# Kernel optimization log

Hardware: AMD Instinct MI355X
Metric: run time of the kernel (lower is better)

Reference implementation:

```python
import jax, jax.numpy as jnp
import numpy as np

N, E = 10000, 160000
IN_DIM, HID, HEADS, EDGE_DIM = 1024, 1024, 8, 4
HEAD_DIM = HID // HEADS  # 128
NEG_SLOPE = 0.2
EPS = 1e-16  # PyG softmax denominator epsilon


def _lin(key, fan_in, fan_out, bias=True):
    kw, kb = jax.random.split(key)
    s = 1.0 / np.sqrt(fan_in)
    W = jax.random.uniform(kw, (fan_in, fan_out), minval=-s, maxval=s, dtype=jnp.float32)
    if not bias:
        return W
    b = jax.random.uniform(kb, (fan_out,), minval=-s, maxval=s, dtype=jnp.float32)
    return W, b


def setup_inputs() -> dict:
    key = jax.random.key(0)
    ks = jax.random.split(key, 24)
    x = jax.random.normal(ks[0], (N, IN_DIM), dtype=jnp.float32)
    edge_index = jax.random.randint(ks[1], (2, E), 0, N, dtype=jnp.int64)
    edge_attr = jax.random.normal(ks[2], (E, EDGE_DIM), dtype=jnp.float32)

    W_in, b_in = _lin(ks[3], IN_DIM, HID)

    def gat_params(k):
        k0, k1, k2, k3, k4 = jax.random.split(k, 5)
        Wl, bl = _lin(k0, HID, HID)
        Wr, br = _lin(k1, HID, HID)
        We = _lin(k2, EDGE_DIM, HID, bias=False)
        att = jax.random.normal(k3, (HEADS, HEAD_DIM), dtype=jnp.float32) / np.sqrt(HEAD_DIM)
        b = jnp.zeros((HID,), dtype=jnp.float32)
        return Wl, bl, Wr, br, We, att, b

    g1 = gat_params(ks[4])
    g2 = gat_params(ks[5])
    m1_W, m1_b = _lin(ks[6], HID, 512)
    m2_W, m2_b = _lin(ks[7], 512, 128)
    m3_W, m3_b = _lin(ks[8], 128, 1)

    names1 = ['g1_Wl', 'g1_bl', 'g1_Wr', 'g1_br', 'g1_We', 'g1_att', 'g1_b']
    names2 = ['g2_Wl', 'g2_bl', 'g2_Wr', 'g2_br', 'g2_We', 'g2_att', 'g2_b']
    out = {'x': x, 'edge_index': edge_index, 'edge_attr': edge_attr,
           'W_in': W_in, 'b_in': b_in,
           'm1_W': m1_W, 'm1_b': m1_b, 'm2_W': m2_W, 'm2_b': m2_b,
           'm3_W': m3_W, 'm3_b': m3_b}
    out.update(dict(zip(names1, g1)))
    out.update(dict(zip(names2, g2)))
    return out


def gatv2_layer(x, src, dst, edge_attr, Wl, bl, Wr, br, We, att, bias):
    # x: [N, HID]; returns [N, HID] (heads concatenated)
    xl = (x @ Wl + bl).reshape(-1, HEADS, HEAD_DIM)  # source transform
    xr = (x @ Wr + br).reshape(-1, HEADS, HEAD_DIM)  # target transform
    e = (edge_attr @ We).reshape(-1, HEADS, HEAD_DIM)
    m = jax.nn.leaky_relu(xl[src] + xr[dst] + e, NEG_SLOPE)  # [E, H, D]
    logits = jnp.einsum('ehd,hd->eh', m, att)  # [E, H]
    lmax = jax.ops.segment_max(logits, dst, num_segments=N)
    lmax = jnp.where(jnp.isfinite(lmax), lmax, 0.0)
    ex = jnp.exp(logits - lmax[dst])
    denom = jax.ops.segment_sum(ex, dst, num_segments=N)
    alpha = ex / (denom[dst] + EPS)  # [E, H]
    out = jax.ops.segment_sum(xl[src] * alpha[..., None], dst, num_segments=N)
    return out.reshape(-1, HID) + bias


def reference(x, edge_index, edge_attr, W_in, b_in,
              g1_Wl, g1_bl, g1_Wr, g1_br, g1_We, g1_att, g1_b,
              g2_Wl, g2_bl, g2_Wr, g2_br, g2_We, g2_att, g2_b,
              m1_W, m1_b, m2_W, m2_b, m3_W, m3_b):
    src, dst = edge_index[0], edge_index[1]
    h = jax.nn.elu(x @ W_in + b_in)
    h = jax.nn.elu(gatv2_layer(h, src, dst, edge_attr, g1_Wl, g1_bl, g1_Wr, g1_br, g1_We, g1_att, g1_b))
    h = jax.nn.elu(gatv2_layer(h, src, dst, edge_attr, g2_Wl, g2_bl, g2_Wr, g2_br, g2_We, g2_att, g2_b))
    h = jax.nn.relu(h @ m1_W + m1_b)
    h = jax.nn.relu(h @ m2_W + m2_b)
    return jax.nn.sigmoid(h @ m3_W + m3_b)  # [N, 1]
```

## Files before the change

kernel.cpp:

```cpp
#include <hip/hip_runtime.h>
#include <math.h>

constexpr int HID = 1024;
constexpr float NEG_SLOPE = 0.2f;
constexpr float EPSV = 1e-16f;

typedef __bf16 bf16x8 __attribute__((ext_vector_type(8)));
typedef float f32x4 __attribute__((ext_vector_type(4)));
typedef float f32x2 __attribute__((ext_vector_type(2)));
typedef unsigned short us8 __attribute__((ext_vector_type(8)));
typedef unsigned short us4 __attribute__((ext_vector_type(4)));
typedef unsigned short ushort_t;

#define AS1 __attribute__((address_space(1)))
#define AS3 __attribute__((address_space(3)))

__device__ __forceinline__ float4 ld4(const float* p){ return *reinterpret_cast<const float4*>(p); }
__device__ __forceinline__ float b2f(ushort_t u){ return __uint_as_float(((unsigned)u) << 16); }
__device__ __forceinline__ ushort_t f2b(float f){
  unsigned u = __float_as_uint(f);
  return (ushort_t)((u + 0x7FFFu + ((u >> 16) & 1u)) >> 16);
}
__device__ __forceinline__ float rfl(float x){
  return __uint_as_float(__builtin_amdgcn_readfirstlane(__float_as_uint(x)));
}
__device__ __forceinline__ f32x2 up2(unsigned u){
  f32x2 r;
  r[0] = __uint_as_float(u << 16);
  r[1] = __uint_as_float(u & 0xffff0000u);
  return r;
}
__device__ __forceinline__ f32x2 lrelu2(f32x2 v){
  return __builtin_elementwise_max(v, v * NEG_SLOPE);
}

struct TP5 { const float* src[5]; ushort_t* dst[5]; };
__global__ __launch_bounds__(256) void transpose_f2b_5(TP5 p){
  const int z = blockIdx.z;
  const float* W = p.src[z];
  ushort_t* WT = p.dst[z];
  __shared__ float tile[32][33];
  const int tx = threadIdx.x & 31, ty = threadIdx.x >> 5;
  const int n0 = blockIdx.x * 32, k0 = blockIdx.y * 32;
  #pragma unroll
  for (int r = 0; r < 32; r += 8)
    tile[ty + r][tx] = W[(size_t)(k0 + ty + r) * 1024 + n0 + tx];
  __syncthreads();
  #pragma unroll
  for (int r = 0; r < 32; r += 8)
    WT[(size_t)(n0 + ty + r) * 1024 + k0 + tx] = f2b(tile[tx][ty + r]);
}

__global__ __launch_bounds__(256) void transpose_f2b(const float* __restrict__ W, ushort_t* __restrict__ WT,
                                                     int K, int N){
  __shared__ float tile[32][33];
  const int tx = threadIdx.x & 31, ty = threadIdx.x >> 5;
  const int n0 = blockIdx.x * 32, k0 = blockIdx.y * 32;
  #pragma unroll
  for (int r = 0; r < 32; r += 8)
    tile[ty + r][tx] = W[(size_t)(k0 + ty + r) * N + n0 + tx];
  __syncthreads();
  #pragma unroll
  for (int r = 0; r < 32; r += 8)
    WT[(size_t)(n0 + ty + r) * K + k0 + tx] = f2b(tile[tx][ty + r]);
}

struct BC4 { const float* s[4]; };
__global__ void concat_bias(BC4 p, float* __restrict__ dst){
  const int i = blockIdx.x * blockDim.x + threadIdx.x;
  dst[i] = p.s[i >> 10][i & 1023];
}

__global__ void convert_f2b(const float* __restrict__ in, ushort_t* __restrict__ out, size_t n){
  size_t i = ((size_t)blockIdx.x * blockDim.x + threadIdx.x) * 4;
  const size_t stride = (size_t)gridDim.x * blockDim.x * 4;
  for (; i < n; i += stride){
    const float4 v = ld4(in + i);
    us4 o = {f2b(v.x), f2b(v.y), f2b(v.z), f2b(v.w)};
    *reinterpret_cast<us4*>(out + i) = o;
  }
}

template<int ACT, int OUTB>
__global__ __launch_bounds__(512, 4) void gemm_mfma(
    const ushort_t* __restrict__ A, const ushort_t* __restrict__ BT,
    const float* __restrict__ bias, float* __restrict__ Cf, ushort_t* __restrict__ Cb,
    int M, int K, int N)
{
  __shared__ __align__(16) char smem[65536];
  ushort_t* Asl = (ushort_t*)smem;
  ushort_t* Bsl = (ushort_t*)(smem + 32768);
  const int tid = threadIdx.x;
  const int lane = tid & 63, wave = tid >> 6;
  const int wr = (wave >> 1) * 32;
  const int wc = (wave & 1) * 64;

  const int nwg = gridDim.x * gridDim.y;
  int wg = blockIdx.y * gridDim.x + blockIdx.x;
  {
    const int q = nwg >> 3, r = nwg & 7;
    const int xcd = wg & 7, lo = wg >> 3;
    wg = (xcd < r ? xcd * (q + 1) : r * (q + 1) + (xcd - r) * q) + lo;
  }
  const int bm = (wg / gridDim.x) * 128, bn = (wg % gridDim.x) * 128;

  const int mrow = lane & 15;
  const int r0 = (lane >> 4) * 4;

  f32x4 acc[2][4];
  #pragma unroll
  for (int i = 0; i < 2; ++i)
    #pragma unroll
    for (int j = 0; j < 4; ++j)
      acc[i][j] = (f32x4){0.f, 0.f, 0.f, 0.f};

  const int srow = tid >> 3;
  const int ssl = (((lane & 7) ^ (lane >> 3))) * 8;
  const int ldst = wave * 512 + lane * 8;

  auto stage = [&](int buf, int k0){
    #pragma unroll
    for (int q = 0; q < 2; ++q){
      const int row = q * 64 + srow;
      int arow = bm + row; if (arow > M - 1) arow = M - 1;
      __builtin_amdgcn_global_load_lds(
        (const AS1 unsigned int*)(A + (size_t)arow * K + k0 + ssl),
        (AS3 unsigned int*)(Asl + buf * 8192 + q * 4096 + ldst), 16, 0, 0);
      __builtin_amdgcn_global_load_lds(
        (const AS1 unsigned int*)(BT + (size_t)(bn + row) * K + k0 + ssl),
        (AS3 unsigned int*)(Bsl + buf * 8192 + q * 4096 + ldst), 16, 0, 0);
    }
  };

  const int kslice = (lane >> 4);
  auto compute = [&](int buf){
    #pragma unroll
    for (int ks = 0; ks < 2; ++ks){
      bf16x8 af[2], bfr[4];
      #pragma unroll
      for (int i = 0; i < 2; ++i){
        const int row = wr + i * 16 + mrow;
        const int sl = (ks * 4 + kslice) ^ (row & 7);
        af[i] = *reinterpret_cast<const bf16x8*>(&Asl[buf * 8192 + row * 64 + sl * 8]);
      }
      #pragma unroll
      for (int j = 0; j < 4; ++j){
        const int row = wc + j * 16 + mrow;
        const int sl = (ks * 4 + kslice) ^ (row & 7);
        bfr[j] = *reinterpret_cast<const bf16x8*>(&Bsl[buf * 8192 + row * 64 + sl * 8]);
      }
      #pragma unroll
      for (int i = 0; i < 2; ++i)
        #pragma unroll
        for (int j = 0; j < 4; ++j)
          acc[i][j] = __builtin_amdgcn_mfma_f32_16x16x32_bf16(af[i], bfr[j], acc[i][j], 0, 0, 0);
    }
  };

  const int NT = K >> 6;
  stage(0, 0);
  if (NT > 1) stage(1, 64);

  int cur = 0;
  for (int t = 0; t < NT; ++t){
    if (t + 1 < NT) asm volatile("s_waitcnt vmcnt(4)" ::: "memory");
    else            asm volatile("s_waitcnt vmcnt(0)" ::: "memory");
    __builtin_amdgcn_s_barrier();
    compute(cur);
    __builtin_amdgcn_s_barrier();
    if (t + 2 < NT) stage(cur, (t + 2) << 6);
    cur ^= 1;
  }

  float* ldsF = (float*)smem;
  const int wbase = wave * 2048;
  #pragma unroll
  for (int i = 0; i < 2; ++i)
    #pragma unroll
    for (int j = 0; j < 4; ++j)
      #pragma unroll
      for (int r = 0; r < 4; ++r)
        ldsF[wbase + (i * 16 + r0 + r) * 64 + j * 16 + mrow] = acc[i][j][r];
  asm volatile("s_waitcnt lgkmcnt(0)" ::: "memory");

  const int lrow = lane >> 3, lcol = (lane & 7) * 8;
  #pragma unroll
  for (int i2 = 0; i2 < 4; ++i2){
    const int row = bm + wr + i2 * 8 + lrow;
    const int col = bn + wc + lcol;
    if (row < M){
      const f32x4 lo = *reinterpret_cast<const f32x4*>(&ldsF[wbase + (i2 * 8 + lrow) * 64 + lcol]);
      const f32x4 hi = *reinterpret_cast<const f32x4*>(&ldsF[wbase + (i2 * 8 + lrow) * 64 + lcol + 4]);
      const float4 b0 = ld4(bias + col), b1 = ld4(bias + col + 4);
      float v[8] = {lo[0] + b0.x, lo[1] + b0.y, lo[2] + b0.z, lo[3] + b0.w,
                    hi[0] + b1.x, hi[1] + b1.y, hi[2] + b1.z, hi[3] + b1.w};
      #pragma unroll
      for (int u = 0; u < 8; ++u){
        float t2 = v[u];
        if (ACT == 1) t2 = fmaxf(t2, 0.f);
        else if (ACT == 2) t2 = (t2 > 0.f) ? t2 : expm1f(t2);
        v[u] = t2;
      }
      if (OUTB){
        us8 ov;
        #pragma unroll
        for (int u = 0; u < 8; ++u) ov[u] = f2b(v[u]);
        *reinterpret_cast<us8*>(Cb + (size_t)row * N + col) = ov;
      } else {
        *reinterpret_cast<float4*>(Cf + (size_t)row * N + col)     = make_float4(v[0], v[1], v[2], v[3]);
        *reinterpret_cast<float4*>(Cf + (size_t)row * N + col + 4) = make_float4(v[4], v[5], v[6], v[7]);
      }
    }
  }
}

__global__ void count_deg(const int* __restrict__ dst, int* __restrict__ deg, int E){
  int e = blockIdx.x * blockDim.x + threadIdx.x;
  if (e < E) atomicAdd(&deg[dst[e]], 1);
}

__global__ __launch_bounds__(1024) void scan_offsets(const int* __restrict__ deg, int* __restrict__ offs, int n){
  __shared__ int ws[16];
  const int tid = threadIdx.x, lane = tid & 63, wid = tid >> 6;
  int running = 0;
  for (int base = 0; base < n; base += 1024){
    const int i = base + tid;
    const int v = (i < n) ? deg[i] : 0;
    int x = v;
    #pragma unroll
    for (int s = 1; s < 64; s <<= 1){
      int u = __shfl_up(x, s, 64);
      if (lane >= s) x += u;
    }
    if (lane == 63) ws[wid] = x;
    __syncthreads();
    if (tid < 16){
      int p = ws[tid];
      #pragma unroll
      for (int s = 1; s < 16; s <<= 1){
        int u = __shfl_up(p, s, 64);
        if (tid >= s) p += u;
      }
      ws[tid] = p;
    }
    __syncthreads();
    const int wpre = (wid > 0) ? ws[wid - 1] : 0;
    if (i < n) offs[i] = running + wpre + x - v;
    running += ws[15];
    __syncthreads();
  }
  if (tid == 0) offs[n] = running;
}

__global__ void fill_csr(const int* __restrict__ src, const int* __restrict__ dst,
                         const float* __restrict__ edge_attr,
                         const int* __restrict__ offs, int* __restrict__ cursor,
                         int* __restrict__ csr_src, float* __restrict__ csr_ea, int E){
  int e = blockIdx.x * blockDim.x + threadIdx.x;
  if (e < E){
    int d = dst[e];
    int pos = offs[d] + atomicAdd(&cursor[d], 1);
    csr_src[pos] = src[e];
    *reinterpret_cast<float4*>(csr_ea + (size_t)pos * 4) = ld4(edge_attr + (size_t)e * 4);
  }
}

__global__ __launch_bounds__(128) void fused_gat(
    const int* __restrict__ offs, const int* __restrict__ csr_src, const float* __restrict__ csr_ea,
    const float* __restrict__ We, const float* __restrict__ att,
    const ushort_t* __restrict__ xlr, const float* __restrict__ bias,
    ushort_t* __restrict__ out, int N)
{
  const int n = blockIdx.x;
  const int t = threadIdx.x;
  const int d0 = t * 8;

  f32x2 W0[4], W1[4], W2[4], W3[4], AT[4];
  #pragma unroll
  for (int q = 0; q < 4; ++q){
    W0[q] = *reinterpret_cast<const f32x2*>(We + d0 + 2*q);
    W1[q] = *reinterpret_cast<const f32x2*>(We + 1024 + d0 + 2*q);
    W2[q] = *reinterpret_cast<const f32x2*>(We + 2048 + d0 + 2*q);
    W3[q] = *reinterpret_cast<const f32x2*>(We + 3072 + d0 + 2*q);
    AT[q] = *reinterpret_cast<const f32x2*>(att + d0 + 2*q);
  }
  f32x2 xr[4];
  {
    const uint4 xu = *reinterpret_cast<const uint4*>(xlr + (size_t)n * 2048 + 1024 + d0);
    xr[0] = up2(xu.x); xr[1] = up2(xu.y); xr[2] = up2(xu.z); xr[3] = up2(xu.w);
  }

  const int o0 = __builtin_amdgcn_readfirstlane(offs[n]);
  const int o1 = __builtin_amdgcn_readfirstlane(offs[n + 1]);

  f32x2 acc[4];
  #pragma unroll
  for (int q = 0; q < 4; ++q) acc[q] = (f32x2){0.f, 0.f};
  float lsum = 0.f, mcur = -1e30f;

  uint4 xa = {0u,0u,0u,0u}, xb = {0u,0u,0u,0u};
  float eA0=0.f,eA1=0.f,eA2=0.f,eA3=0.f, eB0=0.f,eB1=0.f,eB2=0.f,eB3=0.f;

  auto ldedge = [&](int idx, uint4& xv, float& e0, float& e1, float& e2, float& e3){
    const int s = __builtin_amdgcn_readfirstlane(csr_src[idx]);
    xv = *reinterpret_cast<const uint4*>(xlr + (size_t)s * 2048 + d0);
    const float4 e = ld4(csr_ea + (size_t)idx * 4);
    e0 = rfl(e.x); e1 = rfl(e.y); e2 = rfl(e.z); e3 = rfl(e.w);
  };

  if (o0 < o1)     ldedge(o0,     xa, eA0,eA1,eA2,eA3);
  if (o0 + 1 < o1) ldedge(o0 + 1, xb, eB0,eB1,eB2,eB3);

  int i = o0;
  while (i < o1){
    const uint4 ca = xa; const float a0=eA0,a1=eA1,a2=eA2,a3=eA3;
    const uint4 cb = xb; const float b0=eB0,b1=eB1,b2=eB2,b3=eB3;
    const bool pair = (i + 1 < o1);
    const int ni = i + 2;
    if (ni < o1)     ldedge(ni,     xa, eA0,eA1,eA2,eA3);
    if (ni + 1 < o1) ldedge(ni + 1, xb, eB0,eB1,eB2,eB3);

    f32x2 xav[4] = {up2(ca.x), up2(ca.y), up2(ca.z), up2(ca.w)};
    f32x2 xbv[4] = {up2(cb.x), up2(cb.y), up2(cb.z), up2(cb.w)};

    f32x2 za2 = {0.f,0.f}, zb2 = {0.f,0.f};
    #pragma unroll
    for (int q = 0; q < 4; ++q){
      f32x2 ma = xav[q] + xr[q];
      ma += W0[q]*a0; ma += W1[q]*a1; ma += W2[q]*a2; ma += W3[q]*a3;
      ma = lrelu2(ma);
      za2 += ma * AT[q];
      f32x2 mb = xbv[q] + xr[q];
      mb += W0[q]*b0; mb += W1[q]*b1; mb += W2[q]*b2; mb += W3[q]*b3;
      mb = lrelu2(mb);
      zb2 += mb * AT[q];
    }
    float zA = za2[0] + za2[1];
    float zB = zb2[0] + zb2[1];
    #pragma unroll
    for (int sh = 1; sh <= 8; sh <<= 1){
      zA += __shfl_xor(zA, sh, 64);
      zB += __shfl_xor(zB, sh, 64);
    }

    if (pair){
      const float mn = fmaxf(fmaxf(mcur, zA), zB);
      const float sc = __expf(mcur - mn);
      const float pA = __expf(zA - mn);
      const float pB = __expf(zB - mn);
      lsum = lsum * sc + pA + pB;
      #pragma unroll
      for (int q = 0; q < 4; ++q)
        acc[q] = acc[q] * sc + xav[q] * pA + xbv[q] * pB;
      mcur = mn;
    } else {
      const float mn = fmaxf(mcur, zA);
      const float sc = __expf(mcur - mn);
      const float pA = __expf(zA - mn);
      lsum = lsum * sc + pA;
      #pragma unroll
      for (int q = 0; q < 4; ++q)
        acc[q] = acc[q] * sc + xav[q] * pA;
      mcur = mn;
    }
    i = ni;
  }

  const float r = 1.f / (lsum + EPSV);
  const float4 bv0 = ld4(bias + d0);
  const float4 bv1 = ld4(bias + d0 + 4);
  float o_[8] = {acc[0][0]*r + bv0.x, acc[0][1]*r + bv0.y, acc[1][0]*r + bv0.z, acc[1][1]*r + bv0.w,
                 acc[2][0]*r + bv1.x, acc[2][1]*r + bv1.y, acc[3][0]*r + bv1.z, acc[3][1]*r + bv1.w};
  us8 ov;
  #pragma unroll
  for (int j = 0; j < 8; ++j){
    float v = o_[j];
    v = (v > 0.f) ? v : expm1f(v);
    ov[j] = f2b(v);
  }
  *reinterpret_cast<us8*>(out + (size_t)n * HID + d0) = ov;
}

__global__ __launch_bounds__(256) void mlp_final(const float* __restrict__ h, const float* __restrict__ w,
                                                 const float* __restrict__ b, float* __restrict__ out, int M)
{
  const int row = (int)((blockIdx.x * (size_t)blockDim.x + threadIdx.x) >> 6);
  const int lane = threadIdx.x & 63;
  if (row >= M) return;
  const float2 v  = *reinterpret_cast<const float2*>(&h[(size_t)row * 128 + lane * 2]);
  const float2 ww = *reinterpret_cast<const float2*>(&w[lane * 2]);
  float s = v.x * ww.x + v.y * ww.y;
  #pragma unroll
  for (int m = 1; m <= 32; m <<= 1) s += __shfl_xor(s, m, 64);
  if (lane == 0) out[row] = 1.f / (1.f + expf(-(s + b[0])));
}

extern "C" void kernel_launch(void* const* d_in, const int* in_sizes, int n_in,
                              void* d_out, int out_size, void* d_ws, size_t ws_size,
                              hipStream_t stream)
{
  const float* x        = (const float*)d_in[0];
  const int*   ei       = (const int*)d_in[1];
  const float* edge_attr= (const float*)d_in[2];
  const float* W_in     = (const float*)d_in[3];
  const float* b_in     = (const float*)d_in[4];
  const float* m1_W     = (const float*)d_in[5];
  const float* m1_b     = (const float*)d_in[6];
  const float* m2_W     = (const float*)d_in[7];
  const float* m2_b     = (const float*)d_in[8];
  const float* m3_W     = (const float*)d_in[9];
  const float* m3_b     = (const float*)d_in[10];
  const float* g_Wl[2]  = {(const float*)d_in[11], (const float*)d_in[18]};
  const float* g_bl[2]  = {(const float*)d_in[12], (const float*)d_in[19]};
  const float* g_Wr[2]  = {(const float*)d_in[13], (const float*)d_in[20]};
  const float* g_br[2]  = {(const float*)d_in[14], (const float*)d_in[21]};
  const float* g_We[2]  = {(const float*)d_in[15], (const float*)d_in[22]};
  const float* g_att[2] = {(const float*)d_in[16], (const float*)d_in[23]};
  const float* g_b[2]   = {(const float*)d_in[17], (const float*)d_in[24]};

  const int Nn = in_sizes[0] / 1024;
  const int E  = in_sizes[1] / 2;
  const int* srcv = ei;
  const int* dstv = ei + E;
  float* out = (float*)d_out;

  char* wsp = (char*)d_ws;
  size_t off = 0;
  auto alloc = [&](size_t bytes)->char* {
    char* p = wsp + off;
    off = (off + bytes + 255) & ~(size_t)255;
    return p;
  };
  ushort_t* hbf  = (ushort_t*)alloc((size_t)Nn * HID * 2);
  ushort_t* ubuf = (ushort_t*)alloc((size_t)Nn * HID * 2);
  ushort_t* xlr  = (ushort_t*)alloc((size_t)Nn * 2048 * 2);
  float*    m2f  = (float*)   alloc((size_t)Nn * 128 * 4);
  ushort_t* WinT = (ushort_t*)alloc((size_t)1024 * 1024 * 2);
  ushort_t* Wlr0 = (ushort_t*)alloc((size_t)2048 * 1024 * 2);
  ushort_t* Wlr1 = (ushort_t*)alloc((size_t)2048 * 1024 * 2);
  ushort_t* m1T  = (ushort_t*)alloc((size_t)512 * 1024 * 2);
  ushort_t* m2T  = (ushort_t*)alloc((size_t)128 * 512 * 2);
  float*  biasc  = (float*)   alloc((size_t)2048 * 2 * 4);
  int* deg    = (int*)alloc((size_t)Nn * 2 * 4);
  int* cursor = deg + Nn;
  int* offs   = (int*)alloc((size_t)(Nn + 1) * 4);
  int* csr_src= (int*)alloc((size_t)E * 4);
  float* csr_ea = (float*)alloc((size_t)E * 4 * 4);
  ushort_t* Wlr[2]  = {Wlr0, Wlr1};
  float*    blr[2]  = {biasc, biasc + 2048};

  TP5 tp;
  tp.src[0] = W_in;    tp.dst[0] = WinT;
  tp.src[1] = g_Wl[0]; tp.dst[1] = Wlr0;
  tp.src[2] = g_Wr[0]; tp.dst[2] = Wlr0 + 1024*1024;
  tp.src[3] = g_Wl[1]; tp.dst[3] = Wlr1;
  tp.src[4] = g_Wr[1]; tp.dst[4] = Wlr1 + 1024*1024;
  transpose_f2b_5<<<dim3(32, 32, 5), 256, 0, stream>>>(tp);
  transpose_f2b<<<dim3(16, 32), 256, 0, stream>>>(m1_W, m1T, 1024, 512);
  transpose_f2b<<<dim3(4, 16), 256, 0, stream>>>(m2_W, m2T, 512, 128);
  convert_f2b<<<2048, 256, 0, stream>>>(x, ubuf, (size_t)Nn * HID);
  BC4 bc; bc.s[0] = g_bl[0]; bc.s[1] = g_br[0]; bc.s[2] = g_bl[1]; bc.s[3] = g_br[1];
  concat_bias<<<16, 256, 0, stream>>>(bc, biasc);

  hipMemsetAsync(deg, 0, (size_t)Nn * 2 * 4, stream);
  count_deg<<<(E + 255)/256, 256, 0, stream>>>(dstv, deg, E);
  scan_offsets<<<1, 1024, 0, stream>>>(deg, offs, Nn);
  fill_csr<<<(E + 255)/256, 256, 0, stream>>>(srcv, dstv, edge_attr, offs, cursor, csr_src, csr_ea, E);

  const int MB = (Nn + 127) / 128;
  gemm_mfma<2, 1><<<dim3(8, MB), 512, 0, stream>>>(ubuf, WinT, b_in, nullptr, hbf, Nn, 1024, 1024);

  for (int L = 0; L < 2; ++L){
    gemm_mfma<0, 1><<<dim3(16, MB), 512, 0, stream>>>(hbf, Wlr[L], blr[L], nullptr, xlr, Nn, 1024, 2048);
    fused_gat<<<Nn, 128, 0, stream>>>(offs, csr_src, csr_ea, g_We[L], g_att[L], xlr, g_b[L], hbf, Nn);
  }

  gemm_mfma<1, 1><<<dim3(4, MB), 512, 0, stream>>>(hbf, m1T, m1_b, nullptr, ubuf, Nn, 1024, 512);
  gemm_mfma<1, 0><<<dim3(1, MB), 512, 0, stream>>>(ubuf, m2T, m2_b, m2f, nullptr, Nn, 512, 128);
  mlp_final<<<((size_t)Nn * 64 + 255)/256, 256, 0, stream>>>(m2f, m3_W, m3_b, out, Nn);
}
```

Before: 336.7 us.

## Stage edge indices and attributes in LDS and prefetch four gathers ahead

The fused GAT aggregation kernel now loads each chunk of up to 64 CSR source indices and edge attributes into shared memory cooperatively. It then walks the chunk four edges at a time, prefetching the next four source rows from global memory. The goal is to keep more gather loads in flight and to take the per-edge scalar index and attribute loads off the dependency chain. The cost is two block barriers per chunk, more registers for the extra in-flight rows, and wasted loads on tail edges that are clamped to the last valid one.

```diff
diff --git a/kernel.cpp b/kernel.cpp
--- a/kernel.cpp
+++ b/kernel.cpp
@@ -271,6 +271,9 @@
     const ushort_t* __restrict__ xlr, const float* __restrict__ bias,
     ushort_t* __restrict__ out, int N)
 {
+  __shared__ int Ssrc[64];
+  __shared__ __align__(16) float Sea[64 * 4];
+
   const int n = blockIdx.x;
   const int t = threadIdx.x;
   const int d0 = t * 8;
@@ -298,72 +301,112 @@
   for (int q = 0; q < 4; ++q) acc[q] = (f32x2){0.f, 0.f};
   float lsum = 0.f, mcur = -1e30f;
 
-  uint4 xa = {0u,0u,0u,0u}, xb = {0u,0u,0u,0u};
-  float eA0=0.f,eA1=0.f,eA2=0.f,eA3=0.f, eB0=0.f,eB1=0.f,eB2=0.f,eB3=0.f;
-
-  auto ldedge = [&](int idx, uint4& xv, float& e0, float& e1, float& e2, float& e3){
-    const int s = __builtin_amdgcn_readfirstlane(csr_src[idx]);
-    xv = *reinterpret_cast<const uint4*>(xlr + (size_t)s * 2048 + d0);
-    const float4 e = ld4(csr_ea + (size_t)idx * 4);
-    e0 = rfl(e.x); e1 = rfl(e.y); e2 = rfl(e.z); e3 = rfl(e.w);
-  };
-
-  if (o0 < o1)     ldedge(o0,     xa, eA0,eA1,eA2,eA3);
-  if (o0 + 1 < o1) ldedge(o0 + 1, xb, eB0,eB1,eB2,eB3);
-
-  int i = o0;
-  while (i < o1){
-    const uint4 ca = xa; const float a0=eA0,a1=eA1,a2=eA2,a3=eA3;
-    const uint4 cb = xb; const float b0=eB0,b1=eB1,b2=eB2,b3=eB3;
-    const bool pair = (i + 1 < o1);
-    const int ni = i + 2;
-    if (ni < o1)     ldedge(ni,     xa, eA0,eA1,eA2,eA3);
-    if (ni + 1 < o1) ldedge(ni + 1, xb, eB0,eB1,eB2,eB3);
-
-    f32x2 xav[4] = {up2(ca.x), up2(ca.y), up2(ca.z), up2(ca.w)};
-    f32x2 xbv[4] = {up2(cb.x), up2(cb.y), up2(cb.z), up2(cb.w)};
-
-    f32x2 za2 = {0.f,0.f}, zb2 = {0.f,0.f};
-    #pragma unroll
-    for (int q = 0; q < 4; ++q){
-      f32x2 ma = xav[q] + xr[q];
-      ma += W0[q]*a0; ma += W1[q]*a1; ma += W2[q]*a2; ma += W3[q]*a3;
-      ma = lrelu2(ma);
-      za2 += ma * AT[q];
-      f32x2 mb = xbv[q] + xr[q];
-      mb += W0[q]*b0; mb += W1[q]*b1; mb += W2[q]*b2; mb += W3[q]*b3;
-      mb = lrelu2(mb);
-      zb2 += mb * AT[q];
-    }
-    float zA = za2[0] + za2[1];
-    float zB = zb2[0] + zb2[1];
-    #pragma unroll
-    for (int sh = 1; sh <= 8; sh <<= 1){
-      zA += __shfl_xor(zA, sh, 64);
-      zB += __shfl_xor(zB, sh, 64);
-    }
-
-    if (pair){
-      const float mn = fmaxf(fmaxf(mcur, zA), zB);
-      const float sc = __expf(mcur - mn);
-      const float pA = __expf(zA - mn);
-      const float pB = __expf(zB - mn);
-      lsum = lsum * sc + pA + pB;
-      #pragma unroll
-      for (int q = 0; q < 4; ++q)
-        acc[q] = acc[q] * sc + xav[q] * pA + xbv[q] * pB;
-      mcur = mn;
-    } else {
-      const float mn = fmaxf(mcur, zA);
-      const float sc = __expf(mcur - mn);
-      const float pA = __expf(zA - mn);
-      lsum = lsum * sc + pA;
-      #pragma unroll
-      for (int q = 0; q < 4; ++q)
-        acc[q] = acc[q] * sc + xav[q] * pA;
-      mcur = mn;
-    }
-    i = ni;
+  for (int c0 = o0; c0 < o1; c0 += 64){
+    const int m = (o1 - c0 < 64) ? (o1 - c0) : 64;
+    __syncthreads();
+    if (t < m){
+      Ssrc[t] = csr_src[c0 + t];
+      *reinterpret_cast<float4*>(&Sea[t * 4]) = ld4(csr_ea + (size_t)(c0 + t) * 4);
+    }
+    __syncthreads();
+
+    auto gather = [&](int j)->uint4{
+      const int jj = (j < m) ? j : (m - 1);
+      const int s = __builtin_amdgcn_readfirstlane(Ssrc[jj]);
+      return *reinterpret_cast<const uint4*>(xlr + (size_t)s * 2048 + d0);
+    };
+
+    uint4 p0 = gather(0), p1 = gather(1), p2 = gather(2), p3 = gather(3);
+
+    for (int j = 0; j < m; j += 4){
+      const uint4 ca = p0, cb = p1, cc = p2, cd = p3;
+      if (j + 4 < m){
+        p0 = gather(j + 4); p1 = gather(j + 5); p2 = gather(j + 6); p3 = gather(j + 7);
+      }
+      const int jB = (j + 1 < m) ? j + 1 : m - 1;
+      const int jC = (j + 2 < m) ? j + 2 : m - 1;
+      const int jD = (j + 3 < m) ? j + 3 : m - 1;
+      const float4 eA = *reinterpret_cast<const float4*>(&Sea[j  * 4]);
+      const float4 eB = *reinterpret_cast<const float4*>(&Sea[jB * 4]);
+      const float4 eC = *reinterpret_cast<const float4*>(&Sea[jC * 4]);
+      const float4 eD = *reinterpret_cast<const float4*>(&Sea[jD * 4]);
+
+      f32x2 xa[4] = {up2(ca.x), up2(ca.y), up2(ca.z), up2(ca.w)};
+      f32x2 xb[4] = {up2(cb.x), up2(cb.y), up2(cb.z), up2(cb.w)};
+      f32x2 xc[4] = {up2(cc.x), up2(cc.y), up2(cc.z), up2(cc.w)};
+      f32x2 xd[4] = {up2(cd.x), up2(cd.y), up2(cd.z), up2(cd.w)};
+
+      f32x2 sA = {0.f,0.f}, sB = {0.f,0.f}, sC = {0.f,0.f}, sD = {0.f,0.f};
+      #pragma unroll
+      for (int q = 0; q < 4; ++q){
+        f32x2 mA = xa[q] + xr[q];
+        mA += W0[q]*eA.x; mA += W1[q]*eA.y; mA += W2[q]*eA.z; mA += W3[q]*eA.w;
+        sA += lrelu2(mA) * AT[q];
+        f32x2 mB = xb[q] + xr[q];
+        mB += W0[q]*eB.x; mB += W1[q]*eB.y; mB += W2[q]*eB.z; mB += W3[q]*eB.w;
+        sB += lrelu2(mB) * AT[q];
+        f32x2 mC = xc[q] + xr[q];
+        mC += W0[q]*eC.x; mC += W1[q]*eC.y; mC += W2[q]*eC.z; mC += W3[q]*eC.w;
+        sC += lrelu2(mC) * AT[q];
+        f32x2 mD = xd[q] + xr[q];
+        mD += W0[q]*eD.x; mD += W1[q]*eD.y; mD += W2[q]*eD.z; mD += W3[q]*eD.w;
+        sD += lrelu2(mD) * AT[q];
+      }
+      float zA = sA[0] + sA[1];
+      float zB = sB[0] + sB[1];
+      float zC = sC[0] + sC[1];
+      float zD = sD[0] + sD[1];
+      #pragma unroll
+      for (int sh = 1; sh <= 8; sh <<= 1){
+        zA += __shfl_xor(zA, sh, 64);
+        zB += __shfl_xor(zB, sh, 64);
+        zC += __shfl_xor(zC, sh, 64);
+        zD += __shfl_xor(zD, sh, 64);
+      }
+
+      if (j + 1 < m){
+        const float mn = fmaxf(fmaxf(mcur, zA), zB);
+        const float sc = __expf(mcur - mn);
+        const float pA = __expf(zA - mn);
+        const float pB = __expf(zB - mn);
+        lsum = lsum * sc + pA + pB;
+        #pragma unroll
+        for (int q = 0; q < 4; ++q)
+          acc[q] = acc[q] * sc + xa[q] * pA + xb[q] * pB;
+        mcur = mn;
+      } else {
+        const float mn = fmaxf(mcur, zA);
+        const float sc = __expf(mcur - mn);
+        const float pA = __expf(zA - mn);
+        lsum = lsum * sc + pA;
+        #pragma unroll
+        for (int q = 0; q < 4; ++q)
+          acc[q] = acc[q] * sc + xa[q] * pA;
+        mcur = mn;
+      }
+      if (j + 2 < m){
+        if (j + 3 < m){
+          const float mn = fmaxf(fmaxf(mcur, zC), zD);
+          const float sc = __expf(mcur - mn);
+          const float pC = __expf(zC - mn);
+          const float pD = __expf(zD - mn);
+          lsum = lsum * sc + pC + pD;
+          #pragma unroll
+          for (int q = 0; q < 4; ++q)
+            acc[q] = acc[q] * sc + xc[q] * pC + xd[q] * pD;
+          mcur = mn;
+        } else {
+          const float mn = fmaxf(mcur, zC);
+          const float sc = __expf(mcur - mn);
+          const float pC = __expf(zC - mn);
+          lsum = lsum * sc + pC;
+          #pragma unroll
+          for (int q = 0; q < 4; ++q)
+            acc[q] = acc[q] * sc + xc[q] * pC;
+          mcur = mn;
+        }
+      }
+    }
   }
 
   const float r = 1.f / (lsum + EPSV);
```

After: 343.9 us. +2.1%, slower.
